# Performance work log

Hardware: AMD Instinct MI355X
Metric: run time of the kernel (lower is better)

## Reference

```python
import jax, jax.numpy as jnp
import numpy as np

D_MODEL = 256
N_HEAD = 8
D_FF = 2048
B, N = 8, 1024
NEG = -9e15
EPS = 1e-5


def _layernorm(x, g, b):
    mu = jnp.mean(x, axis=-1, keepdims=True)
    var = jnp.mean(jnp.square(x - mu), axis=-1, keepdims=True)
    return (x - mu) * jax.lax.rsqrt(var + EPS) * g + b


def setup_inputs() -> dict:
    key = jax.random.key(0)
    ks = jax.random.split(key, 12)
    d, dff = D_MODEL, D_FF
    s = 1.0 / np.sqrt(d)
    inp = {
        "src": jax.random.normal(ks[0], (B, N, d), dtype=jnp.float32),
        "adj": jax.random.randint(ks[1], (B, N, N), 0, 2, dtype=jnp.int32),
        "W_gat": jax.random.normal(ks[2], (d, d), dtype=jnp.float32) * s,
        "a_gat": jax.random.normal(ks[3], (2 * d, 1), dtype=jnp.float32) * s,
        "in_proj_w": jax.random.normal(ks[4], (3 * d, d), dtype=jnp.float32) * s,
        "in_proj_b": jnp.zeros((3 * d,), dtype=jnp.float32),
        "out_proj_w": jax.random.normal(ks[5], (d, d), dtype=jnp.float32) * s,
        "out_proj_b": jnp.zeros((d,), dtype=jnp.float32),
        "lin1_w": jax.random.normal(ks[6], (dff, d), dtype=jnp.float32) * s,
        "lin1_b": jnp.zeros((dff,), dtype=jnp.float32),
        "lin2_w": jax.random.normal(ks[7], (d, dff), dtype=jnp.float32) * (1.0 / np.sqrt(dff)),
        "lin2_b": jnp.zeros((d,), dtype=jnp.float32),
        "ln1_g": jnp.ones((d,), dtype=jnp.float32),
        "ln1_b": jnp.zeros((d,), dtype=jnp.float32),
        "ln2_g": jnp.ones((d,), dtype=jnp.float32),
        "ln2_b": jnp.zeros((d,), dtype=jnp.float32),
        "ln3_g": jnp.ones((d,), dtype=jnp.float32),
        "ln3_b": jnp.zeros((d,), dtype=jnp.float32),
    }
    return inp


def reference(src, adj, W_gat, a_gat, in_proj_w, in_proj_b, out_proj_w, out_proj_b,
              lin1_w, lin1_b, lin2_w, lin2_b, ln1_g, ln1_b, ln2_g, ln2_b, ln3_g, ln3_b):
    d = D_MODEL
    # --- Graph attention (dropout inactive in eval) ---
    Wh = jnp.matmul(src, W_gat)                      # [B,N,d]
    a1 = a_gat[:d, 0]
    a2 = a_gat[d:, 0]
    # e[b,i,j] = Wh_i . a1 + Wh_j . a2  (equivalent to concat+matmul in source)
    f1 = Wh @ a1                                     # [B,N]
    f2 = Wh @ a2                                     # [B,N]
    e = f1[:, :, None] + f2[:, None, :]              # [B,N,N]
    e = jnp.where(adj > 0, e, NEG)
    attn = jax.nn.softmax(e, axis=-1)
    h_prime = jnp.matmul(attn, Wh)                   # [B,N,d]
    graph_out = jax.nn.elu(h_prime)
    x = _layernorm(src + graph_out, ln1_g, ln1_b)

    # --- Multi-head self-attention ---
    qkv = x @ in_proj_w.T + in_proj_b                # [B,N,3d]
    q, k, v = jnp.split(qkv, 3, axis=-1)
    hd = d // N_HEAD
    def heads(t):
        return t.reshape(B, N, N_HEAD, hd).transpose(0, 2, 1, 3)  # [B,H,N,hd]
    q, k, v = heads(q), heads(k), heads(v)
    scores = jnp.einsum("bhid,bhjd->bhij", q, k) / np.sqrt(hd)
    probs = jax.nn.softmax(scores, axis=-1)
    ctx = jnp.einsum("bhij,bhjd->bhid", probs, v)
    ctx = ctx.transpose(0, 2, 1, 3).reshape(B, N, d)
    attn_out = ctx @ out_proj_w.T + out_proj_b
    y = _layernorm(x + attn_out, ln2_g, ln2_b)

    # --- FFN ---
    ff = jax.nn.relu(y @ lin1_w.T + lin1_b) @ lin2_w.T + lin2_b
    return _layernorm(y + ff, ln3_g, ln3_b)
```

## Files before the change

kernel.cpp:

```cpp
#include <hip/hip_runtime.h>
#include <math.h>

constexpr int BATCH = 8;
constexpr int SEQ   = 1024;
constexpr int DM    = 256;
constexpr int DF    = 2048;
constexpr int NH    = 8;
constexpr int HDIM  = 32;
constexpr int ROWS  = BATCH * SEQ;
constexpr float NEGV = -9e15f;
constexpr float EPSV = 1e-5f;
constexpr float QSCALE = 0.2550351822f;
constexpr float LOG2E  = 1.44269504f;

typedef __attribute__((ext_vector_type(8))) short short8;
typedef __attribute__((ext_vector_type(4))) float f32x4;

static __device__ __forceinline__ ushort f2bf(float f) {
    unsigned x = __float_as_uint(f);
    unsigned r = (x + 0x7fffu + ((x >> 16) & 1u)) >> 16;
    return (ushort)r;
}
static __device__ __forceinline__ unsigned cvt_pk_bf16(float lo, float hi) {
    unsigned r;
    asm volatile("v_cvt_pk_bf16_f32 %0, %1, %2" : "=v"(r) : "v"(lo), "v"(hi));
    return r;
}

struct CastArgs {
    const float* in[5];
    ushort* out[5];
    int n4[5];
};
__global__ __launch_bounds__(256) void castall_k(CastArgs a)
{
    int idx = blockIdx.x * 256 + threadIdx.x;
    #pragma unroll
    for (int r = 0; r < 5; r++) {
        if (idx < a.n4[r]) {
            float4 v = *(const float4*)&a.in[r][(size_t)idx * 4];
            ushort4 o; o.x = f2bf(v.x); o.y = f2bf(v.y); o.z = f2bf(v.z); o.w = f2bf(v.w);
            *(ushort4*)&a.out[r][(size_t)idx * 4] = o;
            return;
        }
        idx -= a.n4[r];
    }
}

__global__ __launch_bounds__(256) void tcast_k(const float* __restrict__ In,
                                               ushort* __restrict__ Out,
                                               int R, int C)
{
    __shared__ float Ts[32][33];
    const int r0 = blockIdx.y * 32, c0 = blockIdx.x * 32;
    const int t = threadIdx.x;
    const int lr = t >> 3, lc4 = (t & 7) * 4;
    float4 v = *(const float4*)&In[(size_t)(r0 + lr) * C + c0 + lc4];
    Ts[lr][lc4] = v.x; Ts[lr][lc4 + 1] = v.y; Ts[lr][lc4 + 2] = v.z; Ts[lr][lc4 + 3] = v.w;
    __syncthreads();
    const int oc = t >> 3, or4 = (t & 7) * 4;
    ushort4 o;
    o.x = f2bf(Ts[or4 + 0][oc]); o.y = f2bf(Ts[or4 + 1][oc]);
    o.z = f2bf(Ts[or4 + 2][oc]); o.w = f2bf(Ts[or4 + 3][oc]);
    *(ushort4*)&Out[(size_t)(c0 + oc) * R + r0 + or4] = o;
}

__global__ __launch_bounds__(256) void w12_k(const float* __restrict__ W_gat,
                                             const float* __restrict__ a_gat,
                                             float* __restrict__ w1,
                                             float* __restrict__ w2)
{
    const int t = threadIdx.x;
    const int k = blockIdx.x * 4 + (t >> 6);
    const int l = t & 63;
    float4 wv = *(const float4*)&W_gat[(size_t)k * DM + 4 * l];
    float4 a1 = *(const float4*)&a_gat[4 * l];
    float4 a2 = *(const float4*)&a_gat[DM + 4 * l];
    float s1 = wv.x*a1.x + wv.y*a1.y + wv.z*a1.z + wv.w*a1.w;
    float s2 = wv.x*a2.x + wv.y*a2.y + wv.z*a2.z + wv.w*a2.w;
    #pragma unroll
    for (int off = 32; off; off >>= 1) {
        s1 += __shfl_xor(s1, off, 64);
        s2 += __shfl_xor(s2, off, 64);
    }
    if (l == 0) { w1[k] = s1; w2[k] = s2; }
}

__global__ __launch_bounds__(256) void f12_k(const float* __restrict__ src,
                                             const float* __restrict__ w1,
                                             const float* __restrict__ w2,
                                             float* __restrict__ f1,
                                             float* __restrict__ f2)
{
    const int t = threadIdx.x;
    const size_t row = (size_t)blockIdx.x * 4 + (t >> 6);
    const int l = t & 63;
    float s1 = 0.f, s2 = 0.f;
    #pragma unroll
    for (int i = 0; i < 4; i++) {
        float v = src[row * DM + l + 64*i];
        s1 = fmaf(v, w1[l + 64*i], s1);
        s2 = fmaf(v, w2[l + 64*i], s2);
    }
    #pragma unroll
    for (int off = 32; off; off >>= 1) {
        s1 += __shfl_xor(s1, off, 64);
        s2 += __shfl_xor(s2, off, 64);
    }
    if (l == 0) { f1[row] = s1 * LOG2E; f2[row] = s2 * LOG2E; }
}

template<int EP, int BN>
__global__ __launch_bounds__(256) void gemm_bf(const ushort* __restrict__ A,
                                               const ushort* __restrict__ B,
                                               const float* __restrict__ bias,
                                               float* __restrict__ Cf,
                                               ushort* __restrict__ Cb,
                                               int M, int N, int K, int ldB,
                                               long long sA, long long sB, long long sC)
{
    __shared__ ushort As[128][40];
    __shared__ ushort Bs[BN][40];
    A += (size_t)blockIdx.z * sA;
    B += (size_t)blockIdx.z * sB;

    const int t  = threadIdx.x;
    const int m0 = blockIdx.y * 128, n0 = blockIdx.x * BN;
    const int lane = t & 63, lo = lane & 15, hi = lane >> 4;
    const int w = t >> 6;
    constexpr int NJ = BN / 32;
    const int wr = (w >> 1) * 64;
    const int wc = (w & 1) * (BN / 2);

    const int lrA = t >> 1, lcA = (t & 1) * 16;
    const int lrB = (BN == 128) ? (t >> 1) : (t >> 2);
    const int lcB = (BN == 128) ? ((t & 1) * 16) : ((t & 3) * 8);

    f32x4 acc[4][NJ];
    const f32x4 zero = {0.f, 0.f, 0.f, 0.f};
    #pragma unroll
    for (int i = 0; i < 4; i++)
        #pragma unroll
        for (int j = 0; j < NJ; j++) acc[i][j] = zero;

    const ushort* Ap = A + (size_t)(m0 + lrA) * K + lcA;
    const ushort* Bp = B + (size_t)(n0 + lrB) * ldB + lcB;

    for (int k0 = 0; k0 < K; k0 += 32) {
        short8 a0 = *(const short8*)(Ap + k0);
        short8 a1 = *(const short8*)(Ap + k0 + 8);
        short8 b0 = *(const short8*)(Bp + k0);
        short8 b1;
        if (BN == 128) b1 = *(const short8*)(Bp + k0 + 8);
        __syncthreads();
        *(short8*)&As[lrA][lcA]     = a0;
        *(short8*)&As[lrA][lcA + 8] = a1;
        *(short8*)&Bs[lrB][lcB] = b0;
        if (BN == 128) *(short8*)&Bs[lrB][lcB + 8] = b1;
        __syncthreads();
        short8 afr[4], bfr[NJ];
        #pragma unroll
        for (int i = 0; i < 4; i++) afr[i] = *(const short8*)&As[wr + i*16 + lo][hi * 8];
        #pragma unroll
        for (int j = 0; j < NJ; j++) bfr[j] = *(const short8*)&Bs[wc + j*16 + lo][hi * 8];
        #pragma unroll
        for (int i = 0; i < 4; i++)
            #pragma unroll
            for (int j = 0; j < NJ; j++)
                acc[i][j] = __builtin_amdgcn_mfma_f32_16x16x32_bf16(afr[i], bfr[j], acc[i][j], 0, 0, 0);
    }

    if (EP == 2 || EP == 5 || EP == 6) Cb += (size_t)blockIdx.z * sC;
    else                               Cf += (size_t)blockIdx.z * sC;
    #pragma unroll
    for (int j = 0; j < NJ; j++) {
        const int col = n0 + wc + j * 16 + lo;
        float bj = (EP == 1 || EP == 2 || EP == 6) ? bias[col] : 0.f;
        #pragma unroll
        for (int i = 0; i < 4; i++) {
            const int rbase = m0 + wr + i * 16 + hi * 4;
            #pragma unroll
            for (int r = 0; r < 4; r++) {
                float v = acc[i][j][r] + bj;
                if (EP == 3) v = v > 0.f ? v : expm1f(v);
                if (EP == 2) v = fmaxf(v, 0.f);
                if (EP == 6 && col < DM) v *= QSCALE;
                if (EP == 2 || EP == 5 || EP == 6) Cb[(size_t)(rbase + r) * N + col] = f2bf(v);
                else                               Cf[(size_t)(rbase + r) * N + col] = v;
            }
        }
    }
}

template<bool WB>
__global__ __launch_bounds__(256) void ln_k(const float* __restrict__ a,
                                            const float* __restrict__ r,
                                            const float* __restrict__ g,
                                            const float* __restrict__ be,
                                            float* __restrict__ o,
                                            ushort* __restrict__ ob)
{
    const size_t row = (size_t)blockIdx.x * 4 + (threadIdx.x >> 6);
    const int l = threadIdx.x & 63;
    const float* pa = a + row * DM;
    const float* pr = r + row * DM;
    float v[4]; float s = 0.f;
    #pragma unroll
    for (int i = 0; i < 4; i++) { v[i] = pa[l + 64*i] + pr[l + 64*i]; s += v[i]; }
    #pragma unroll
    for (int off = 32; off; off >>= 1) s += __shfl_xor(s, off, 64);
    float mu = s * (1.0f / DM);
    float q = 0.f;
    #pragma unroll
    for (int i = 0; i < 4; i++) { float d = v[i] - mu; q += d * d; }
    #pragma unroll
    for (int off = 32; off; off >>= 1) q += __shfl_xor(q, off, 64);
    float rs = rsqrtf(q * (1.0f / DM) + EPSV);
    #pragma unroll
    for (int i = 0; i < 4; i++) {
        int c = l + 64*i;
        float out = (v[i] - mu) * rs * g[c] + be[c];
        o[row * DM + c] = out;
        if (WB) ob[row * DM + c] = f2bf(out);
    }
}

__global__ __launch_bounds__(256) void gat_sm_k(const int* __restrict__ adj,
                                                const float* __restrict__ f1,
                                                const float* __restrict__ f2,
                                                ushort* __restrict__ P)
{
    __shared__ float red[8];
    const int i = blockIdx.x, b = i >> 10;
    const int t = threadIdx.x;
    const int4 a4 = *(const int4*)&adj[(size_t)i * SEQ + 4 * t];
    const float4 f4 = *(const float4*)&f2[(size_t)(b << 10) + 4 * t];
    const float f1i = f1[i];
    float e[4];
    e[0] = a4.x > 0 ? f1i + f4.x : NEGV;
    e[1] = a4.y > 0 ? f1i + f4.y : NEGV;
    e[2] = a4.z > 0 ? f1i + f4.z : NEGV;
    e[3] = a4.w > 0 ? f1i + f4.w : NEGV;
    float mx = fmaxf(fmaxf(e[0], e[1]), fmaxf(e[2], e[3]));
    #pragma unroll
    for (int off = 32; off; off >>= 1) mx = fmaxf(mx, __shfl_xor(mx, off, 64));
    if ((t & 63) == 0) red[t >> 6] = mx;
    __syncthreads();
    mx = fmaxf(fmaxf(red[0], red[1]), fmaxf(red[2], red[3]));
    float s = 0.f;
    #pragma unroll
    for (int u = 0; u < 4; u++) { e[u] = exp2f(e[u] - mx); s += e[u]; }
    #pragma unroll
    for (int off = 32; off; off >>= 1) s += __shfl_xor(s, off, 64);
    if ((t & 63) == 0) red[4 + (t >> 6)] = s;
    __syncthreads();
    float inv = 1.0f / (red[4] + red[5] + red[6] + red[7]);
    ushort4 o;
    o.x = f2bf(e[0] * inv); o.y = f2bf(e[1] * inv);
    o.z = f2bf(e[2] * inv); o.w = f2bf(e[3] * inv);
    *(ushort4*)&P[(size_t)i * SEQ + 4 * t] = o;
}

__device__ __forceinline__ int vt_idx(int d, int kv) { return d * 72 + ((d >> 3) & 3) * 16 + kv; }
constexpr int VTSZ = 32 * 72 + 3 * 16 + 8;

__global__ __launch_bounds__(256) void mha_k(const ushort* __restrict__ qkv,
                                             ushort* __restrict__ ctxb)
{
    __shared__ ushort Ks[2][64][40];
    __shared__ ushort Vt[2][VTSZ];
    __shared__ ushort Ps[64][72];

    const int blk = blockIdx.x;
    const int qt = blk & 15, h = (blk >> 4) & 7, b = blk >> 7;
    const int i0 = qt << 6;
    const int t = threadIdx.x;
    const int w = t >> 6, lane = t & 63, lo = lane & 15, hi = lane >> 4;
    const int gsh = lane & 48;
    const size_t base = (size_t)b * SEQ * 768;

    const short8 aQ = *(const short8*)(qkv + base + (size_t)(i0 + 16*w + lo) * 768 + h * HDIM + hi * 8);
    short8 ones;
    #pragma unroll
    for (int e = 0; e < 8; e++) ones[e] = (short)0x3F80;

    const int srow = t >> 2, scb = (t & 3) << 3;
    const int vcol = (srow & 32) | ((srow & 15) << 1) | ((srow >> 4) & 1);
    {
        const ushort* p0 = qkv + base + (size_t)srow * 768 + h * HDIM;
        short8 k0 = *(const short8*)(p0 + 256 + scb);
        short8 v0 = *(const short8*)(p0 + 512 + scb);
        *(short8*)&Ks[0][srow][scb] = k0;
        #pragma unroll
        for (int e = 0; e < 8; e++) Vt[0][vt_idx(scb + e, vcol)] = (ushort)v0[e];
    }

    float m_run[4], l_run[4];
    f32x4 O0 = {0.f, 0.f, 0.f, 0.f}, O1 = {0.f, 0.f, 0.f, 0.f};
    #pragma unroll
    for (int r = 0; r < 4; r++) { m_run[r] = -3.0e38f; l_run[r] = 0.f; }
    const f32x4 zero = {0.f, 0.f, 0.f, 0.f};

    short8 kreg, vreg;
    for (int it = 0; it < 16; it++) {
        const int cur = it & 1;
        if (it < 15) {
            const ushort* nb = qkv + base + (size_t)((it + 1) * 64 + srow) * 768 + h * HDIM;
            kreg = *(const short8*)(nb + 256 + scb);
            vreg = *(const short8*)(nb + 512 + scb);
        }
        __syncthreads();

        f32x4 S[4];
        #pragma unroll
        for (int jt = 0; jt < 4; jt++) {
            short8 bK = *(const short8*)&Ks[cur][16 * jt + lo][hi * 8];
            S[jt] = __builtin_amdgcn_mfma_f32_16x16x32_bf16(aQ, bK, zero, 0, 0, 0);
        }

        float mxl[4];
        bool any = false;
        #pragma unroll
        for (int r = 0; r < 4; r++) {
            mxl[r] = fmaxf(fmaxf(S[0][r], S[1][r]), fmaxf(S[2][r], S[3][r]));
            any = any || (mxl[r] > m_run[r] + 8.f);
        }
        unsigned long long bal = __ballot(any);
        if ((bal >> gsh) & 0xffffULL) {
            #pragma unroll
            for (int r = 0; r < 4; r++) {
                float mx = mxl[r];
                #pragma unroll
                for (int off = 8; off; off >>= 1) mx = fmaxf(mx, __shfl_xor(mx, off, 16));
                float mnew = fmaxf(m_run[r], mx);
                float sc = exp2f(m_run[r] - mnew);
                m_run[r] = mnew;
                l_run[r] *= sc; O0[r] *= sc; O1[r] *= sc;
            }
        }
        #pragma unroll
        for (int r = 0; r < 4; r++) {
            const int row = 16 * w + 4 * hi + r;
            unsigned u01 = cvt_pk_bf16(exp2f(S[0][r] - m_run[r]), exp2f(S[1][r] - m_run[r]));
            unsigned u23 = cvt_pk_bf16(exp2f(S[2][r] - m_run[r]), exp2f(S[3][r] - m_run[r]));
            *(unsigned*)&Ps[row][2 * lo]      = u01;
            *(unsigned*)&Ps[row][32 + 2 * lo] = u23;
        }

        f32x4 O2 = zero;
        #pragma unroll
        for (int kt = 0; kt < 2; kt++) {
            short8 aP  = *(const short8*)&Ps[16 * w + lo][32 * kt + hi * 8];
            short8 bV0 = *(const short8*)&Vt[cur][vt_idx(lo,      32 * kt + hi * 8)];
            short8 bV1 = *(const short8*)&Vt[cur][vt_idx(16 + lo, 32 * kt + hi * 8)];
            O0 = __builtin_amdgcn_mfma_f32_16x16x32_bf16(aP, bV0, O0, 0, 0, 0);
            O1 = __builtin_amdgcn_mfma_f32_16x16x32_bf16(aP, bV1, O1, 0, 0, 0);
            O2 = __builtin_amdgcn_mfma_f32_16x16x32_bf16(aP, ones, O2, 0, 0, 0);
        }
        #pragma unroll
        for (int r = 0; r < 4; r++) l_run[r] += O2[r];

        if (it < 15) {
            *(short8*)&Ks[cur ^ 1][srow][scb] = kreg;
            #pragma unroll
            for (int e = 0; e < 8; e++) Vt[cur ^ 1][vt_idx(scb + e, vcol)] = (ushort)vreg[e];
        }
    }

    #pragma unroll
    for (int r = 0; r < 4; r++) {
        float inv = 1.0f / l_run[r];
        size_t row = (size_t)b * SEQ + i0 + 16 * w + 4 * hi + r;
        ctxb[row * DM + h * HDIM + lo]      = f2bf(O0[r] * inv);
        ctxb[row * DM + h * HDIM + 16 + lo] = f2bf(O1[r] * inv);
    }
}

extern "C" void kernel_launch(void* const* d_in, const int* in_sizes, int n_in,
                              void* d_out, int out_size, void* d_ws, size_t ws_size,
                              hipStream_t stream)
{
    const float* src        = (const float*)d_in[0];
    const int*   adj        = (const int*)  d_in[1];
    const float* W_gat      = (const float*)d_in[2];
    const float* a_gat      = (const float*)d_in[3];
    const float* in_proj_w  = (const float*)d_in[4];
    const float* in_proj_b  = (const float*)d_in[5];
    const float* out_proj_w = (const float*)d_in[6];
    const float* out_proj_b = (const float*)d_in[7];
    const float* lin1_w     = (const float*)d_in[8];
    const float* lin1_b     = (const float*)d_in[9];
    const float* lin2_w     = (const float*)d_in[10];
    const float* lin2_b     = (const float*)d_in[11];
    const float* ln1_g      = (const float*)d_in[12];
    const float* ln1_b_     = (const float*)d_in[13];
    const float* ln2_g      = (const float*)d_in[14];
    const float* ln2_b_     = (const float*)d_in[15];
    const float* ln3_g      = (const float*)d_in[16];
    const float* ln3_b_     = (const float*)d_in[17];

    char* base = (char*)d_ws;
    const size_t MB = 1024 * 1024;
    float*  tmp   = (float*) (base + 0 * MB);
    float*  x     = (float*) (base + 8 * MB);
    float*  y     = (float*) (base + 16 * MB);
    ushort* P_bf  = (ushort*)(base + 24 * MB);
    ushort* qkvb  = (ushort*)(base + 24 * MB);
    ushort* ff1b  = (ushort*)(base + 24 * MB);
    ushort* srcb  = (ushort*)(base + 56 * MB);
    ushort* WhTb  = (ushort*)(base + 60 * MB);
    ushort* xb    = (ushort*)(base + 64 * MB);
    ushort* yb    = (ushort*)(base + 68 * MB);
    ushort* ctxb  = (ushort*)(base + 72 * MB);
    float*  f1    = (float*) (base + 76 * MB);
    float*  f2    = f1 + ROWS;
    float*  w1    = f2 + ROWS;
    float*  w2    = w1 + DM;
    ushort* wgTb  = (ushort*)(base + 77 * MB);
    ushort* ipwb  = wgTb + 65536;
    ushort* opwb  = ipwb + 196608;
    ushort* l1wb  = opwb + 65536;
    ushort* l2wb  = l1wb + 524288;

    dim3 b256(256);

    CastArgs ca;
    ca.in[0] = src;       ca.out[0] = srcb; ca.n4[0] = 2097152 / 4;
    ca.in[1] = in_proj_w; ca.out[1] = ipwb; ca.n4[1] = 196608 / 4;
    ca.in[2] = out_proj_w;ca.out[2] = opwb; ca.n4[2] = 65536 / 4;
    ca.in[3] = lin1_w;    ca.out[3] = l1wb; ca.n4[3] = 524288 / 4;
    ca.in[4] = lin2_w;    ca.out[4] = l2wb; ca.n4[4] = 524288 / 4;
    castall_k<<<(2097152 + 196608 + 65536 + 524288 + 524288) / 4 / 256, b256, 0, stream>>>(ca);
    tcast_k<<<dim3(8, 8), b256, 0, stream>>>(W_gat, wgTb, 256, 256);

    w12_k<<<64, b256, 0, stream>>>(W_gat, a_gat, w1, w2);
    f12_k<<<ROWS / 4, b256, 0, stream>>>(src, w1, w2, f1, f2);
    gemm_bf<5, 64><<<dim3(ROWS/64, 2, 1), b256, 0, stream>>>(wgTb, srcb, nullptr, nullptr, WhTb,
                                                             DM, ROWS, DM, DM, 0, 0, 0);
    gat_sm_k<<<ROWS, b256, 0, stream>>>(adj, f1, f2, P_bf);
    gemm_bf<3, 64><<<dim3(4, 8, 8), b256, 0, stream>>>(P_bf, WhTb, nullptr, tmp, nullptr,
                                                       SEQ, DM, SEQ, ROWS,
                                                       (long long)SEQ * SEQ, (long long)SEQ, (long long)SEQ * DM);
    ln_k<true><<<ROWS / 4, b256, 0, stream>>>(src, tmp, ln1_g, ln1_b_, x, xb);

    gemm_bf<6, 128><<<dim3(6, 64, 1), b256, 0, stream>>>(xb, ipwb, in_proj_b, nullptr, qkvb,
                                                         ROWS, 768, DM, DM, 0, 0, 0);
    mha_k<<<BATCH * NH * (SEQ / 64), b256, 0, stream>>>(qkvb, ctxb);
    gemm_bf<1, 64><<<dim3(4, 64, 1), b256, 0, stream>>>(ctxb, opwb, out_proj_b, tmp, nullptr,
                                                        ROWS, DM, DM, DM, 0, 0, 0);
    ln_k<true><<<ROWS / 4, b256, 0, stream>>>(x, tmp, ln2_g, ln2_b_, y, yb);

    gemm_bf<2, 128><<<dim3(16, 64, 1), b256, 0, stream>>>(yb, l1wb, lin1_b, nullptr, ff1b,
                                                          ROWS, DF, DM, DM, 0, 0, 0);
    gemm_bf<1, 64><<<dim3(4, 64, 1), b256, 0, stream>>>(ff1b, l2wb, lin2_b, tmp, nullptr,
                                                        ROWS, DM, DF, DF, 0, 0, 0);
    ln_k<false><<<ROWS / 4, b256, 0, stream>>>(y, tmp, ln3_g, ln3_b_, (float*)d_out, nullptr);
}
```

Measured before the change: 188.3 us.

## Double-buffer GEMM shared-memory tiles and add BM template for smaller tiles

```diff
diff --git a/kernel.cpp b/kernel.cpp
--- a/kernel.cpp
+++ b/kernel.cpp
@@ -110,7 +110,7 @@
     if (l == 0) { f1[row] = s1 * LOG2E; f2[row] = s2 * LOG2E; }
 }
 
-template<int EP, int BN>
+template<int EP, int BM, int BN>
 __global__ __launch_bounds__(256) void gemm_bf(const ushort* __restrict__ A,
                                                const ushort* __restrict__ B,
                                                const float* __restrict__ bias,
@@ -119,55 +119,73 @@
                                                int M, int N, int K, int ldB,
                                                long long sA, long long sB, long long sC)
 {
-    __shared__ ushort As[128][40];
-    __shared__ ushort Bs[BN][40];
+    __shared__ ushort As[2][BM][40];
+    __shared__ ushort Bs[2][BN][40];
     A += (size_t)blockIdx.z * sA;
     B += (size_t)blockIdx.z * sB;
 
     const int t  = threadIdx.x;
-    const int m0 = blockIdx.y * 128, n0 = blockIdx.x * BN;
+    const int m0 = blockIdx.y * BM, n0 = blockIdx.x * BN;
     const int lane = t & 63, lo = lane & 15, hi = lane >> 4;
     const int w = t >> 6;
-    constexpr int NJ = BN / 32;
-    const int wr = (w >> 1) * 64;
+    constexpr int NI = BM / 32, NJ = BN / 32;
+    const int wr = (w >> 1) * (BM / 2);
     const int wc = (w & 1) * (BN / 2);
 
-    const int lrA = t >> 1, lcA = (t & 1) * 16;
+    const int lrA = (BM == 128) ? (t >> 1) : (t >> 2);
+    const int lcA = (BM == 128) ? ((t & 1) * 16) : ((t & 3) * 8);
     const int lrB = (BN == 128) ? (t >> 1) : (t >> 2);
     const int lcB = (BN == 128) ? ((t & 1) * 16) : ((t & 3) * 8);
 
-    f32x4 acc[4][NJ];
+    f32x4 acc[NI][NJ];
     const f32x4 zero = {0.f, 0.f, 0.f, 0.f};
     #pragma unroll
-    for (int i = 0; i < 4; i++)
+    for (int i = 0; i < NI; i++)
         #pragma unroll
         for (int j = 0; j < NJ; j++) acc[i][j] = zero;
 
     const ushort* Ap = A + (size_t)(m0 + lrA) * K + lcA;
     const ushort* Bp = B + (size_t)(n0 + lrB) * ldB + lcB;
 
-    for (int k0 = 0; k0 < K; k0 += 32) {
-        short8 a0 = *(const short8*)(Ap + k0);
-        short8 a1 = *(const short8*)(Ap + k0 + 8);
-        short8 b0 = *(const short8*)(Bp + k0);
-        short8 b1;
-        if (BN == 128) b1 = *(const short8*)(Bp + k0 + 8);
+    short8 ar0, ar1, br0, br1;
+    ar0 = *(const short8*)(Ap);
+    if constexpr (BM == 128) ar1 = *(const short8*)(Ap + 8);
+    br0 = *(const short8*)(Bp);
+    if constexpr (BN == 128) br1 = *(const short8*)(Bp + 8);
+    *(short8*)&As[0][lrA][lcA] = ar0;
+    if constexpr (BM == 128) *(short8*)&As[0][lrA][lcA + 8] = ar1;
+    *(short8*)&Bs[0][lrB][lcB] = br0;
+    if constexpr (BN == 128) *(short8*)&Bs[0][lrB][lcB + 8] = br1;
+
+    const int NT = K >> 5;
+    for (int it = 0; it < NT; it++) {
+        const int cur = it & 1;
+        if (it + 1 < NT) {
+            const int k0 = (it + 1) << 5;
+            ar0 = *(const short8*)(Ap + k0);
+            if constexpr (BM == 128) ar1 = *(const short8*)(Ap + k0 + 8);
+            br0 = *(const short8*)(Bp + k0);
+            if constexpr (BN == 128) br1 = *(const short8*)(Bp + k0 + 8);
+        }
         __syncthreads();
-        *(short8*)&As[lrA][lcA]     = a0;
-        *(short8*)&As[lrA][lcA + 8] = a1;
-        *(short8*)&Bs[lrB][lcB] = b0;
-        if (BN == 128) *(short8*)&Bs[lrB][lcB + 8] = b1;
-        __syncthreads();
-        short8 afr[4], bfr[NJ];
-        #pragma unroll
-        for (int i = 0; i < 4; i++) afr[i] = *(const short8*)&As[wr + i*16 + lo][hi * 8];
-        #pragma unroll
-        for (int j = 0; j < NJ; j++) bfr[j] = *(const short8*)&Bs[wc + j*16 + lo][hi * 8];
-        #pragma unroll
-        for (int i = 0; i < 4; i++)
+
+        short8 afr[NI], bfr[NJ];
+        #pragma unroll
+        for (int i = 0; i < NI; i++) afr[i] = *(const short8*)&As[cur][wr + i*16 + lo][hi * 8];
+        #pragma unroll
+        for (int j = 0; j < NJ; j++) bfr[j] = *(const short8*)&Bs[cur][wc + j*16 + lo][hi * 8];
+        #pragma unroll
+        for (int i = 0; i < NI; i++)
             #pragma unroll
             for (int j = 0; j < NJ; j++)
                 acc[i][j] = __builtin_amdgcn_mfma_f32_16x16x32_bf16(afr[i], bfr[j], acc[i][j], 0, 0, 0);
+
+        if (it + 1 < NT) {
+            *(short8*)&As[cur ^ 1][lrA][lcA] = ar0;
+            if constexpr (BM == 128) *(short8*)&As[cur ^ 1][lrA][lcA + 8] = ar1;
+            *(short8*)&Bs[cur ^ 1][lrB][lcB] = br0;
+            if constexpr (BN == 128) *(short8*)&Bs[cur ^ 1][lrB][lcB + 8] = br1;
+        }
     }
 
     if (EP == 2 || EP == 5 || EP == 6) Cb += (size_t)blockIdx.z * sC;
@@ -177,7 +195,7 @@
         const int col = n0 + wc + j * 16 + lo;
         float bj = (EP == 1 || EP == 2 || EP == 6) ? bias[col] : 0.f;
         #pragma unroll
-        for (int i = 0; i < 4; i++) {
+        for (int i = 0; i < NI; i++) {
             const int rbase = m0 + wr + i * 16 + hi * 4;
             #pragma unroll
             for (int r = 0; r < 4; r++) {
@@ -435,24 +453,24 @@
 
     w12_k<<<64, b256, 0, stream>>>(W_gat, a_gat, w1, w2);
     f12_k<<<ROWS / 4, b256, 0, stream>>>(src, w1, w2, f1, f2);
-    gemm_bf<5, 64><<<dim3(ROWS/64, 2, 1), b256, 0, stream>>>(wgTb, srcb, nullptr, nullptr, WhTb,
-                                                             DM, ROWS, DM, DM, 0, 0, 0);
+    gemm_bf<5, 64, 64><<<dim3(ROWS/64, DM/64, 1), b256, 0, stream>>>(wgTb, srcb, nullptr, nullptr, WhTb,
+                                                                     DM, ROWS, DM, DM, 0, 0, 0);
     gat_sm_k<<<ROWS, b256, 0, stream>>>(adj, f1, f2, P_bf);
-    gemm_bf<3, 64><<<dim3(4, 8, 8), b256, 0, stream>>>(P_bf, WhTb, nullptr, tmp, nullptr,
-                                                       SEQ, DM, SEQ, ROWS,
-                                                       (long long)SEQ * SEQ, (long long)SEQ, (long long)SEQ * DM);
+    gemm_bf<3, 64, 64><<<dim3(DM/64, SEQ/64, 8), b256, 0, stream>>>(P_bf, WhTb, nullptr, tmp, nullptr,
+                                                                    SEQ, DM, SEQ, ROWS,
+                                                                    (long long)SEQ * SEQ, (long long)SEQ, (long long)SEQ * DM);
     ln_k<true><<<ROWS / 4, b256, 0, stream>>>(src, tmp, ln1_g, ln1_b_, x, xb);
 
-    gemm_bf<6, 128><<<dim3(6, 64, 1), b256, 0, stream>>>(xb, ipwb, in_proj_b, nullptr, qkvb,
-                                                         ROWS, 768, DM, DM, 0, 0, 0);
+    gemm_bf<6, 128, 128><<<dim3(6, 64, 1), b256, 0, stream>>>(xb, ipwb, in_proj_b, nullptr, qkvb,
+                                                              ROWS, 768, DM, DM, 0, 0, 0);
     mha_k<<<BATCH * NH * (SEQ / 64), b256, 0, stream>>>(qkvb, ctxb);
-    gemm_bf<1, 64><<<dim3(4, 64, 1), b256, 0, stream>>>(ctxb, opwb, out_proj_b, tmp, nullptr,
-                                                        ROWS, DM, DM, DM, 0, 0, 0);
+    gemm_bf<1, 64, 64><<<dim3(DM/64, ROWS/64, 1), b256, 0, stream>>>(ctxb, opwb, out_proj_b, tmp, nullptr,
+                                                                     ROWS, DM, DM, DM, 0, 0, 0);
     ln_k<true><<<ROWS / 4, b256, 0, stream>>>(x, tmp, ln2_g, ln2_b_, y, yb);
 
-    gemm_bf<2, 128><<<dim3(16, 64, 1), b256, 0, stream>>>(yb, l1wb, lin1_b, nullptr, ff1b,
-                                                          ROWS, DF, DM, DM, 0, 0, 0);
-    gemm_bf<1, 64><<<dim3(4, 64, 1), b256, 0, stream>>>(ff1b, l2wb, lin2_b, tmp, nullptr,
-                                                        ROWS, DM, DF, DF, 0, 0, 0);
+    gemm_bf<2, 128, 128><<<dim3(16, 64, 1), b256, 0, stream>>>(yb, l1wb, lin1_b, nullptr, ff1b,
+                                                               ROWS, DF, DM, DM, 0, 0, 0);
+    gemm_bf<1, 64, 64><<<dim3(DM/64, ROWS/64, 1), b256, 0, stream>>>(ff1b, l2wb, lin2_b, tmp, nullptr,
+                                                                     ROWS, DM, DF, DF, 0, 0, 0);
     ln_k<false><<<ROWS / 4, b256, 0, stream>>>(y, tmp, ln3_g, ln3_b_, (float*)d_out, nullptr);
 }
```

After: 167.0 us. 11.3% less time.
